# Optimization experiments

Measured on AMD Instinct MI355X. Metric: run time of the kernel, lower is better.

The kernel has to match this reference:

```python
import jax, jax.numpy as jnp
import numpy as np

B, C, H, W = 16, 256, 32, 32
NUM_LAYERS = 30
OUT = 16  # sqrt(out_channels)
EPS = 1e-5


def setup_inputs() -> dict:
    key = jax.random.key(0)
    k1, k2, k3 = jax.random.split(key, 3)
    x = jax.random.normal(k1, (B, C, H, W), dtype=jnp.float32)
    # delta_t ~ small positive values (module inits ~N(0.01, 0.005))
    delta_t = jax.random.uniform(k2, (NUM_LAYERS, 1), dtype=jnp.float32) * 0.02
    matrices = jax.random.normal(k3, (NUM_LAYERS, 1, 1, OUT, OUT), dtype=jnp.float32) * 0.1
    gamma = jnp.ones((H * W,), dtype=jnp.float32)   # BatchNorm2d weight, oc = i*i = H*W
    beta = jnp.zeros((H * W,), dtype=jnp.float32)   # BatchNorm2d bias
    return {"x": x, "delta_t": delta_t, "matrices": matrices, "gamma": gamma, "beta": beta}


def _bn_relu6(z, gamma, beta):
    # training-mode BatchNorm2d over channel axis 1 (channels = H*W), then ReLU6
    mean = jnp.mean(z, axis=(0, 2, 3), keepdims=True)
    var = jnp.mean(jnp.square(z - mean), axis=(0, 2, 3), keepdims=True)  # biased var
    zhat = (z - mean) * jax.lax.rsqrt(var + EPS)
    g = gamma.reshape(1, -1, 1, 1)
    b = beta.reshape(1, -1, 1, 1)
    return jnp.clip(zhat * g + b, 0.0, 6.0)


def reference(x, delta_t, matrices, gamma, beta):
    b, c, h, w = x.shape
    hw = h * w
    # feature_reshape: [B,C,H,W] -> [B,HW,C] -> [B,HW,out,out] (inn == out branch)
    x1 = x.reshape(b, c, hw).transpose(0, 2, 1).reshape(b, hw, OUT, OUT)
    dt = jnp.clip(delta_t, 0.0, 6.0)[:, 0]  # relu6(delta_t), shape [L]

    def step(y0, params):
        m, dtl = params  # m: [1,1,out,out] broadcasts elementwise against x1
        dydt = -y0 + _bn_relu6(y0 + m * x1, gamma, beta)
        return y0 + dtl * dydt, None

    y0, _ = jax.lax.scan(step, x1, (matrices, dt))
    # (y0 + x1): [B, HW, out, out] -> view [B,H,W,out*out] -> permute to [B,out*out,H,W]
    y = (y0 + x1).reshape(b, h, w, OUT * OUT).transpose(0, 3, 1, 2)
    return y
```

## Files before the change

kernel.cpp:

```cpp
#include <hip/hip_runtime.h>

typedef float v2f __attribute__((ext_vector_type(2)));

#define HW      1024
#define NLAYERS 30
#define TPB     256

template <int CTRL, int RMASK>
__device__ __forceinline__ float dpp_add(float x) {
    int t = __builtin_amdgcn_update_dpp(0, __builtin_bit_cast(int, x),
                                        CTRL, RMASK, 0xf, true);
    return x + __builtin_bit_cast(float, t);
}
__device__ __forceinline__ float wave_sum64(float x) {
    x = dpp_add<0x111, 0xf>(x);
    x = dpp_add<0x112, 0xf>(x);
    x = dpp_add<0x114, 0xf>(x);
    x = dpp_add<0x118, 0xf>(x);
    x = dpp_add<0x142, 0xa>(x);
    x = dpp_add<0x143, 0xc>(x);
    return x;
}

__global__ __launch_bounds__(TPB) void ode_fused(const float* __restrict__ x,
                                                 const float* __restrict__ delta_t,
                                                 const float* __restrict__ matrices,
                                                 const float* __restrict__ gamma,
                                                 const float* __restrict__ beta,
                                                 float* __restrict__ out) {
    const int bid = blockIdx.x;
    const int p   = ((bid & 7) << 7) | (bid >> 3);
    const int t   = threadIdx.x;

    __shared__ float smat[(NLAYERS + 1) * 256];
    __shared__ float sdt[NLAYERS];
    __shared__ __align__(16) v2f red[2][4];

#pragma unroll
    for (int i = 0; i < NLAYERS; ++i)
        smat[i * 256 + t] = matrices[i * 256 + t];
    if (t < NLAYERS)
        sdt[t] = __builtin_amdgcn_fmed3f(delta_t[t], 0.0f, 6.0f);

    v2f x1[8], y[8];
#pragma unroll
    for (int k = 0; k < 8; ++k) {
        x1[k].x = x[(size_t)(t + 512 * k) * HW + p];
        x1[k].y = x[(size_t)(t + 512 * k + 256) * HW + p];
        y[k] = x1[k];
    }

    const float gp   = gamma[p];
    const float bp   = beta[p];
    const int   wid  = t >> 6;
    const int   lane = t & 63;

    __syncthreads();
    float m_cur = smat[t];

    for (int l = 0; l < NLAYERS; ++l) {
        const float dtl = sdt[l];
        const v2f m2    = {m_cur, m_cur};
        const v2f dt2   = {dtl, dtl};
        const v2f om2   = {1.0f - dtl, 1.0f - dtl};

        v2f z[8];
        v2f sA = {0.f, 0.f}, sB = {0.f, 0.f};
        v2f qA = {0.f, 0.f}, qB = {0.f, 0.f};
#pragma unroll
        for (int k = 0; k < 8; k += 2) {
            z[k]     = __builtin_elementwise_fma(m2, x1[k], y[k]);
            z[k + 1] = __builtin_elementwise_fma(m2, x1[k + 1], y[k + 1]);
            sA += z[k];
            sB += z[k + 1];
            qA = __builtin_elementwise_fma(z[k], z[k], qA);
            qB = __builtin_elementwise_fma(z[k + 1], z[k + 1], qB);
        }
#pragma unroll
        for (int k = 0; k < 8; ++k) y[k] *= om2;

        const v2f sv = sA + sB;
        const v2f qv = qA + qB;
        float s = wave_sum64(sv.x + sv.y);
        float q = wave_sum64(qv.x + qv.y);

        const int par = l & 1;
        if (lane == 63) { v2f w; w.x = s; w.y = q; red[par][wid] = w; }
        m_cur = smat[(l + 1) * 256 + t];
        __syncthreads();

        const float4 r0 = *(const float4*)&red[par][0];
        const float4 r1 = *(const float4*)&red[par][2];
        const float S  = (r0.x + r0.z) + (r1.x + r1.z);
        const float S2 = (r0.y + r0.w) + (r1.y + r1.w);

        const float mean = S * (1.0f / 4096.0f);
        const float var  = fmaf(-mean, mean, S2 * (1.0f / 4096.0f));
        const float rstd = rsqrtf(var + 1e-5f);
        const float g    = gp * rstd;
        const float bb   = fmaf(-mean, g, bp);
        const v2f g2 = {g, g}, b2 = {bb, bb};
        const v2f z0 = {0.f, 0.f}, s6 = {6.f, 6.f};
#pragma unroll
        for (int k = 0; k < 8; ++k) {
            v2f a = __builtin_elementwise_fma(z[k], g2, b2);
            a = __builtin_elementwise_max(a, z0);
            a = __builtin_elementwise_min(a, s6);
            y[k] = __builtin_elementwise_fma(dt2, a, y[k]);
        }
    }

#pragma unroll
    for (int k = 0; k < 8; ++k) {
        out[(size_t)(t + 512 * k) * HW + p]       = y[k].x + x1[k].x;
        out[(size_t)(t + 512 * k + 256) * HW + p] = y[k].y + x1[k].y;
    }
}

extern "C" void kernel_launch(void* const* d_in, const int* in_sizes, int n_in,
                              void* d_out, int out_size, void* d_ws, size_t ws_size,
                              hipStream_t stream) {
    const float* x        = (const float*)d_in[0];
    const float* delta_t  = (const float*)d_in[1];
    const float* matrices = (const float*)d_in[2];
    const float* gamma    = (const float*)d_in[3];
    const float* beta     = (const float*)d_in[4];
    float* out = (float*)d_out;

    ode_fused<<<dim3(HW), dim3(TPB), 0, stream>>>(x, delta_t, matrices, gamma, beta, out);
}
```

Measured before the change: 116.1 us.

## Use one wave per channel to drop LDS reduction and barriers

Each block is now a single 64-thread wave that holds all 4096 elements of its channel in registers (64 floats per thread). The per-layer mean and variance reduction becomes a DPP wave reduction plus readlane broadcast, so the shared-memory exchange and the __syncthreads in every layer are gone. The update is also reformulated algebraically: dt is folded into the affine scale, z is recomputed from y and x1 instead of kept, and the clamp becomes a single med3 against 6*dt. In exchange, register pressure rises sharply and each block has a quarter of the threads, which cuts parallelism per block and may reduce occupancy or cause spills.

```diff
diff --git a/kernel.cpp b/kernel.cpp
--- a/kernel.cpp
+++ b/kernel.cpp
@@ -4,7 +4,6 @@
 
 #define HW      1024
 #define NLAYERS 30
-#define TPB     256
 
 template <int CTRL, int RMASK>
 __device__ __forceinline__ float dpp_add(float x) {
@@ -12,109 +11,113 @@
                                         CTRL, RMASK, 0xf, true);
     return x + __builtin_bit_cast(float, t);
 }
-__device__ __forceinline__ float wave_sum64(float x) {
+__device__ __forceinline__ float wave_sum_bcast(float x) {
     x = dpp_add<0x111, 0xf>(x);
     x = dpp_add<0x112, 0xf>(x);
     x = dpp_add<0x114, 0xf>(x);
     x = dpp_add<0x118, 0xf>(x);
     x = dpp_add<0x142, 0xa>(x);
     x = dpp_add<0x143, 0xc>(x);
-    return x;
+    return __builtin_bit_cast(float,
+        __builtin_amdgcn_readlane(__builtin_bit_cast(int, x), 63));
 }
 
-__global__ __launch_bounds__(TPB) void ode_fused(const float* __restrict__ x,
-                                                 const float* __restrict__ delta_t,
-                                                 const float* __restrict__ matrices,
-                                                 const float* __restrict__ gamma,
-                                                 const float* __restrict__ beta,
-                                                 float* __restrict__ out) {
+__global__ __launch_bounds__(64) void ode_fused(const float* __restrict__ x,
+                                                const float* __restrict__ delta_t,
+                                                const float* __restrict__ matrices,
+                                                const float* __restrict__ gamma,
+                                                const float* __restrict__ beta,
+                                                float* __restrict__ out) {
     const int bid = blockIdx.x;
     const int p   = ((bid & 7) << 7) | (bid >> 3);
     const int t   = threadIdx.x;
 
     __shared__ float smat[(NLAYERS + 1) * 256];
-    __shared__ float sdt[NLAYERS];
-    __shared__ __align__(16) v2f red[2][4];
+    __shared__ float sdt[NLAYERS + 1];
 
 #pragma unroll
-    for (int i = 0; i < NLAYERS; ++i)
-        smat[i * 256 + t] = matrices[i * 256 + t];
+    for (int i = 0; i < NLAYERS * 4; ++i)
+        smat[i * 64 + t] = matrices[i * 64 + t];
     if (t < NLAYERS)
         sdt[t] = __builtin_amdgcn_fmed3f(delta_t[t], 0.0f, 6.0f);
 
-    v2f x1[8], y[8];
+    v2f x1[4][8], y[4][8];
 #pragma unroll
-    for (int k = 0; k < 8; ++k) {
-        x1[k].x = x[(size_t)(t + 512 * k) * HW + p];
-        x1[k].y = x[(size_t)(t + 512 * k + 256) * HW + p];
-        y[k] = x1[k];
-    }
+    for (int c = 0; c < 4; ++c)
+#pragma unroll
+        for (int j = 0; j < 8; ++j) {
+            x1[c][j].x = x[(size_t)(t + 64 * c + 256 * j) * HW + p];
+            x1[c][j].y = x[(size_t)(t + 64 * c + 256 * j + 2048) * HW + p];
+            y[c][j] = x1[c][j];
+        }
 
-    const float gp   = gamma[p];
-    const float bp   = beta[p];
-    const int   wid  = t >> 6;
-    const int   lane = t & 63;
+    const float gp = gamma[p];
+    const float bp = beta[p];
 
     __syncthreads();
-    float m_cur = smat[t];
+
+    float mcur[4];
+#pragma unroll
+    for (int c = 0; c < 4; ++c) mcur[c] = smat[t + 64 * c];
+    float dtl = sdt[0];
 
     for (int l = 0; l < NLAYERS; ++l) {
-        const float dtl = sdt[l];
-        const v2f m2    = {m_cur, m_cur};
-        const v2f dt2   = {dtl, dtl};
-        const v2f om2   = {1.0f - dtl, 1.0f - dtl};
+        v2f sacc[4], qacc[4];
+#pragma unroll
+        for (int i = 0; i < 4; ++i) { sacc[i] = (v2f){0.f, 0.f}; qacc[i] = (v2f){0.f, 0.f}; }
+#pragma unroll
+        for (int c = 0; c < 4; ++c) {
+            const v2f m2 = {mcur[c], mcur[c]};
+#pragma unroll
+            for (int j = 0; j < 8; ++j) {
+                const v2f z = __builtin_elementwise_fma(m2, x1[c][j], y[c][j]);
+                sacc[j & 3] += z;
+                qacc[j & 3] = __builtin_elementwise_fma(z, z, qacc[j & 3]);
+            }
+        }
+        float mnxt[4];
+#pragma unroll
+        for (int c = 0; c < 4; ++c) mnxt[c] = smat[(l + 1) * 256 + t + 64 * c];
+        const float dtn = sdt[l + 1];
 
-        v2f z[8];
-        v2f sA = {0.f, 0.f}, sB = {0.f, 0.f};
-        v2f qA = {0.f, 0.f}, qB = {0.f, 0.f};
-#pragma unroll
-        for (int k = 0; k < 8; k += 2) {
-            z[k]     = __builtin_elementwise_fma(m2, x1[k], y[k]);
-            z[k + 1] = __builtin_elementwise_fma(m2, x1[k + 1], y[k + 1]);
-            sA += z[k];
-            sB += z[k + 1];
-            qA = __builtin_elementwise_fma(z[k], z[k], qA);
-            qB = __builtin_elementwise_fma(z[k + 1], z[k + 1], qB);
-        }
-#pragma unroll
-        for (int k = 0; k < 8; ++k) y[k] *= om2;
-
-        const v2f sv = sA + sB;
-        const v2f qv = qA + qB;
-        float s = wave_sum64(sv.x + sv.y);
-        float q = wave_sum64(qv.x + qv.y);
-
-        const int par = l & 1;
-        if (lane == 63) { v2f w; w.x = s; w.y = q; red[par][wid] = w; }
-        m_cur = smat[(l + 1) * 256 + t];
-        __syncthreads();
-
-        const float4 r0 = *(const float4*)&red[par][0];
-        const float4 r1 = *(const float4*)&red[par][2];
-        const float S  = (r0.x + r0.z) + (r1.x + r1.z);
-        const float S2 = (r0.y + r0.w) + (r1.y + r1.w);
+        const v2f sv = (sacc[0] + sacc[1]) + (sacc[2] + sacc[3]);
+        const v2f qv = (qacc[0] + qacc[1]) + (qacc[2] + qacc[3]);
+        const float S = wave_sum_bcast(sv.x + sv.y);
+        const float Q = wave_sum_bcast(qv.x + qv.y);
 
         const float mean = S * (1.0f / 4096.0f);
-        const float var  = fmaf(-mean, mean, S2 * (1.0f / 4096.0f));
+        const float var  = fmaf(-mean, mean, Q * (1.0f / 4096.0f));
         const float rstd = rsqrtf(var + 1e-5f);
         const float g    = gp * rstd;
         const float bb   = fmaf(-mean, g, bp);
-        const v2f g2 = {g, g}, b2 = {bb, bb};
-        const v2f z0 = {0.f, 0.f}, s6 = {6.f, 6.f};
+        const float gd = g * dtl, bd = bb * dtl, sixdt = 6.0f * dtl;
+        const float om = 1.0f - dtl;
+        const v2f gd2 = {gd, gd}, bd2 = {bd, bd}, om2 = {om, om};
 #pragma unroll
-        for (int k = 0; k < 8; ++k) {
-            v2f a = __builtin_elementwise_fma(z[k], g2, b2);
-            a = __builtin_elementwise_max(a, z0);
-            a = __builtin_elementwise_min(a, s6);
-            y[k] = __builtin_elementwise_fma(dt2, a, y[k]);
+        for (int c = 0; c < 4; ++c) {
+            const float gm = gd * mcur[c];
+            const v2f gm2 = {gm, gm};
+#pragma unroll
+            for (int j = 0; j < 8; ++j) {
+                v2f a = __builtin_elementwise_fma(y[c][j], gd2, bd2);
+                a = __builtin_elementwise_fma(x1[c][j], gm2, a);
+                a.x = __builtin_amdgcn_fmed3f(a.x, 0.0f, sixdt);
+                a.y = __builtin_amdgcn_fmed3f(a.y, 0.0f, sixdt);
+                y[c][j] = __builtin_elementwise_fma(om2, y[c][j], a);
+            }
         }
+#pragma unroll
+        for (int c = 0; c < 4; ++c) mcur[c] = mnxt[c];
+        dtl = dtn;
     }
 
 #pragma unroll
-    for (int k = 0; k < 8; ++k) {
-        out[(size_t)(t + 512 * k) * HW + p]       = y[k].x + x1[k].x;
-        out[(size_t)(t + 512 * k + 256) * HW + p] = y[k].y + x1[k].y;
-    }
+    for (int c = 0; c < 4; ++c)
+#pragma unroll
+        for (int j = 0; j < 8; ++j) {
+            out[(size_t)(t + 64 * c + 256 * j) * HW + p]        = y[c][j].x + x1[c][j].x;
+            out[(size_t)(t + 64 * c + 256 * j + 2048) * HW + p] = y[c][j].y + x1[c][j].y;
+        }
 }
 
 extern "C" void kernel_launch(void* const* d_in, const int* in_sizes, int n_in,
@@ -127,5 +130,5 @@
     const float* beta     = (const float*)d_in[4];
     float* out = (float*)d_out;
 
-    ode_fused<<<dim3(HW), dim3(TPB), 0, stream>>>(x, delta_t, matrices, gamma, beta, out);
+    ode_fused<<<dim3(HW), dim3(64), 0, stream>>>(x, delta_t, matrices, gamma, beta, out);
 }
```

New measurement: 140.3 us. 20.9% more time.
